# Kernel tuning notes

Hardware: AMD Instinct MI355X
Metric: run time of the kernel (lower is better)

Reference implementation:

```python
import jax, jax.numpy as jnp
import numpy as np

N, K, C_S, C_Z, C_G, NUM_RBF = 1024, 32, 384, 128, 16, 64
E = N * K


def _rbf(D):
    # GVP-style radial basis: D_min=0, D_max=20
    D_mu = jnp.linspace(0.0, 20.0, NUM_RBF)
    D_sigma = 20.0 / NUM_RBF
    return jnp.exp(-(((D[..., None] - D_mu) / D_sigma) ** 2))


def _ln(x, g, b, eps=1e-5):
    m = jnp.mean(x, axis=-1, keepdims=True)
    v = jnp.var(x, axis=-1, keepdims=True)
    return (x - m) * jax.lax.rsqrt(v + eps) * g + b


def setup_inputs() -> dict:
    key = jax.random.key(0)
    ks = jax.random.split(key, 16)
    w = lambda k, s: jax.random.normal(k, s, jnp.float32) / np.sqrt(s[0])
    # regular-degree graph: edges grouped by source node (what sparse_to_nested assumes)
    edge_index = jnp.stack([
        jnp.repeat(jnp.arange(N, dtype=jnp.int32), K),
        jax.random.randint(ks[3], (E,), 0, N, dtype=jnp.int32),
    ])
    return {
        "node_features": jax.random.normal(ks[0], (N, C_S), jnp.float32),
        "node_trans": 10.0 * jax.random.normal(ks[1], (N, 3), jnp.float32),
        "edge_features": jax.random.normal(ks[2], (E, C_Z), jnp.float32),
        "edge_index": edge_index,
        "W_nl": w(ks[4], (C_S, C_G)), "b_nl": jnp.zeros((C_G,), jnp.float32),
        "W_nr": w(ks[5], (C_S, C_G)), "b_nr": jnp.zeros((C_G,), jnp.float32),
        "ln_g": jnp.ones((C_Z,), jnp.float32), "ln_b": jnp.zeros((C_Z,), jnp.float32),
        "W_ep": w(ks[6], (C_Z, C_Z)), "b_ep": jnp.zeros((C_Z,), jnp.float32),
        "W_eg": w(ks[7], (C_Z, C_Z)), "b_eg": jnp.zeros((C_Z,), jnp.float32),
        "W_dg": w(ks[8], (C_G * C_G, C_Z)), "b_dg": jnp.zeros((C_Z,), jnp.float32),
        "W_dp": w(ks[9], (NUM_RBF, C_Z)), "b_dp": jnp.zeros((C_Z,), jnp.float32),
        "lno_g": jnp.ones((C_Z,), jnp.float32), "lno_b": jnp.zeros((C_Z,), jnp.float32),
        "W_lo": w(ks[10], (C_Z, C_Z)), "b_lo": jnp.zeros((C_Z,), jnp.float32),
        "W_og": w(ks[11], (C_Z, C_Z)), "b_og": jnp.zeros((C_Z,), jnp.float32),
    }


def reference(node_features, node_trans, edge_features, edge_index,
              W_nl, b_nl, W_nr, b_nr, ln_g, ln_b, W_ep, b_ep, W_eg, b_eg,
              W_dg, b_dg, W_dp, b_dp, lno_g, lno_b, W_lo, b_lo, W_og, b_og):
    n = node_features.shape[0]
    e = edge_index.shape[1]
    k = e // n
    cz = edge_features.shape[-1]
    eps = 1e-8
    nl = node_features @ W_nl + b_nl            # [N, cg]
    nr = node_features @ W_nr + b_nr            # [N, cg]
    # node_left[edge_index[0]] grouped by source node is constant within a group,
    # so edge3 = outer(nl[n], nr[n]) broadcast over (i, j)
    outer = nl[:, :, None] * nr[:, None, :]     # [N, cg, cg] ; flatten order = (a*cg + b)
    gate3 = jax.nn.sigmoid(outer.reshape(n, -1) @ W_dg + b_dg)   # [N, cz]
    dst = edge_index[1].reshape(n, k)           # [N, K]
    t = node_trans[dst]                         # [N, K, 3]
    diff = t[:, None, :, :] - t[:, :, None, :] + eps             # t[n,j] - t[n,i] + eps
    dist = jnp.sqrt(jnp.sum(diff * diff, axis=-1))               # [N, K, K]
    d3 = jnp.einsum('nijr,rz->nijz', _rbf(dist), W_dp) + b_dp    # [N, K, K, cz]
    e3 = gate3[:, None, None, :] * d3                            # sigmoid(dist_gate) * dist_proj
    ef = _ln(edge_features.reshape(n, k, cz), ln_g, ln_b)        # [N, K, cz]
    e2 = jax.nn.sigmoid(ef @ W_eg + b_eg) * (ef @ W_ep + b_ep)   # [N, K, cz]
    upd = jnp.einsum('nijz,njz->niz', e3, e2)                    # triangle multiply over j
    upd = _ln(upd, lno_g, lno_b) @ W_lo + b_lo
    upd = upd * jax.nn.sigmoid(ef @ W_og + b_og)                 # out gate
    return upd.reshape(e, cz)
```

## Files before the change

kernel.cpp:

```cpp
#include <hip/hip_runtime.h>

#define NN 1024
#define KK 32
#define CZ 128
#define CS 384
#define CG 16
#define NR 64

typedef __attribute__((ext_vector_type(8)))  _Float16 f16x8;
typedef __attribute__((ext_vector_type(16))) float    f32x16;

__device__ __forceinline__ float sigmoidf_(float x) { return 1.0f / (1.0f + __expf(-x)); }

__device__ __forceinline__ unsigned short h_bits(float f) {
    _Float16 h = (_Float16)f;
    return __builtin_bit_cast(unsigned short, h);
}
__device__ __forceinline__ float h2f_bits(unsigned short b) {
    return (float)__builtin_bit_cast(_Float16, b);
}

__launch_bounds__(256, 2)
__global__ void ntmu_kernel(
    const float* __restrict__ nf,
    const float* __restrict__ ntr,
    const float* __restrict__ efeat,
    const int*   __restrict__ eidx,
    const float* __restrict__ W_nl, const float* __restrict__ b_nl,
    const float* __restrict__ W_nr, const float* __restrict__ b_nr,
    const float* __restrict__ ln_g, const float* __restrict__ ln_b,
    const float* __restrict__ W_ep, const float* __restrict__ b_ep,
    const float* __restrict__ W_eg, const float* __restrict__ b_eg,
    const float* __restrict__ W_dg, const float* __restrict__ b_dg,
    const float* __restrict__ W_dp, const float* __restrict__ b_dp,
    const float* __restrict__ lno_g, const float* __restrict__ lno_b,
    const float* __restrict__ W_lo, const float* __restrict__ b_lo,
    const float* __restrict__ W_og, const float* __restrict__ b_og,
    float* __restrict__ out)
{
    const int n    = blockIdx.x;
    const int tid  = threadIdx.x;
    const int lane = tid & 63;
    const int wave = tid >> 6;
    const int hi   = lane >> 5;
    const int zt   = wave * 32;
    const int zc   = zt + (lane & 31);
    const int ebase = n * KK;

    __shared__ float s_e2 [KK*CZ];
    __shared__ float s_upd[KK*CZ];
    __shared__ short s_og [KK*CZ];
    __shared__ short s_ef [KK*CZ];
    __shared__ short s_updb[KK*CZ];
    __shared__ __align__(16) short s_T[4*KK*NR];
    __shared__ float s_t[KK][4];
    __shared__ float s_gate3[CZ];
    __shared__ float s_nl[CG], s_nr[CG];
    __shared__ float s_pp[2][CZ];

    if (tid < KK) {
        int d = eidx[NN*KK + ebase + tid];
        s_t[tid][0] = ntr[d*3 + 0];
        s_t[tid][1] = ntr[d*3 + 1];
        s_t[tid][2] = ntr[d*3 + 2];
    }
    if (wave < 2) {
        const float* W  = (wave == 0) ? W_nl : W_nr;
        const float* bb = (wave == 0) ? b_nl : b_nr;
        int g = lane >> 2, q = lane & 3;
        const float* x = nf + n * CS;
        float s = 0.f;
        int c0 = q * 96;
        for (int c = c0; c < c0 + 96; ++c) s = fmaf(x[c], W[c*CG + g], s);
        s += __shfl_xor(s, 1);
        s += __shfl_xor(s, 2);
        if (q == 0) { if (wave == 0) s_nl[g] = s + bb[g]; else s_nr[g] = s + bb[g]; }
    }
    __syncthreads();

    {
        int z = tid & 127, h = tid >> 7;
        float p = 0.f;
        for (int a = h*8; a < h*8 + 8; ++a) {
            float nla = s_nl[a];
            #pragma unroll
            for (int b = 0; b < 16; ++b)
                p = fmaf(nla * s_nr[b], W_dg[(a*16 + b)*CZ + z], p);
        }
        s_pp[h][z] = p;
    }

    {
        float g0 = ln_g[lane], g1 = ln_g[lane + 64];
        float bb0 = ln_b[lane], bb1 = ln_b[lane + 64];
        for (int it = 0; it < 8; ++it) {
            int j = it*4 + wave;
            const float* row = efeat + (ebase + j) * CZ;
            float x0 = row[lane], x1 = row[lane + 64];
            float s = x0 + x1, s2 = x0*x0 + x1*x1;
            #pragma unroll
            for (int o = 1; o < 64; o <<= 1) { s += __shfl_xor(s, o); s2 += __shfl_xor(s2, o); }
            float mu  = s * (1.f/128.f);
            float inv = rsqrtf(s2 * (1.f/128.f) - mu*mu + 1e-5f);
            float y0 = (x0 - mu) * inv * g0 + bb0;
            float y1 = (x1 - mu) * inv * g1 + bb1;
            int swz = (j & 7) << 4;
            *(short*)((char*)s_ef + ((j*256 + lane*2)        ^ swz)) = (short)h_bits(y0);
            *(short*)((char*)s_ef + ((j*256 + (lane+64)*2)   ^ swz)) = (short)h_bits(y1);
        }
    }
    __syncthreads();

    if (tid < CZ) s_gate3[tid] = sigmoidf_(s_pp[0][tid] + s_pp[1][tid] + b_dg[tid]);

    f32x16 aEp, aEg, aOg;
    #pragma unroll
    for (int r = 0; r < 16; ++r) { aEp[r] = 0.f; aEg[r] = 0.f; aOg[r] = 0.f; }
    {
        const int arow = lane & 31;
        const int aswz = (arow & 7) << 4;
        for (int ks = 0; ks < 8; ++ks) {
            int abyte = (arow*256 + ks*32 + hi*16) ^ aswz;
            f16x8 af = *reinterpret_cast<const f16x8*>((const char*)s_ef + abyte);
            int c0 = ks*16 + hi*8;
            const float* pep = W_ep + c0*CZ + zc;
            const float* peg = W_eg + c0*CZ + zc;
            const float* pog = W_og + c0*CZ + zc;
            f16x8 bep, beg, bog;
            #pragma unroll
            for (int t = 0; t < 8; ++t) {
                bep[t] = (_Float16)pep[t*CZ];
                beg[t] = (_Float16)peg[t*CZ];
                bog[t] = (_Float16)pog[t*CZ];
            }
            aEp = __builtin_amdgcn_mfma_f32_32x32x16_f16(af, bep, aEp, 0, 0, 0);
            aEg = __builtin_amdgcn_mfma_f32_32x32x16_f16(af, beg, aEg, 0, 0, 0);
            aOg = __builtin_amdgcn_mfma_f32_32x32x16_f16(af, bog, aOg, 0, 0, 0);
        }
    }
    float esum = 0.f;
    {
        float bep = b_ep[zc], beg = b_eg[zc], bogc = b_og[zc];
        #pragma unroll
        for (int r = 0; r < 16; ++r) {
            int j = (r & 3) + 8*(r >> 2) + 4*hi;
            float e2v = sigmoidf_(aEg[r] + beg) * (aEp[r] + bep);
            s_e2[j*CZ + zc] = e2v;
            esum += e2v;
            s_og[j*CZ + zc] = (short)h_bits(sigmoidf_(aOg[r] + bogc));
        }
        esum += __shfl_xor(esum, 32);
    }

    f16x8 wdp[4];
    #pragma unroll
    for (int ks = 0; ks < 4; ++ks) {
        int c0 = ks*16 + hi*8;
        const float* p = W_dp + c0*CZ + zc;
        #pragma unroll
        for (int t = 0; t < 8; ++t) wdp[ks][t] = (_Float16)p[t*CZ];
    }
    __syncthreads();
    const float g3  = s_gate3[zc];
    const float bdp = b_dp[zc];

    const float spacing     = 20.0f / 63.0f;
    const float inv_spacing = 63.0f / 20.0f;
    const float inv_sigma   = 64.0f / 20.0f;
    for (int ch = 0; ch < 8; ++ch) {
        __syncthreads();
        if (tid < 128) {
            int il = tid >> 5, j = tid & 31;
            int i  = ch*4 + il;
            float dx = s_t[j][0] - s_t[i][0] + 1e-8f;
            float dy = s_t[j][1] - s_t[i][1] + 1e-8f;
            float dz = s_t[j][2] - s_t[i][2] + 1e-8f;
            float D  = sqrtf(dx*dx + dy*dy + dz*dz);
            int idx = (int)(D * inv_spacing);
            int r0  = min(max((idx - 3) & ~1, 0), 56);
            int rowbyte = (il*KK + j) * 128;
            int swz = (j & 7) << 4;
            int4 zz; zz.x = 0; zz.y = 0; zz.z = 0; zz.w = 0;
            #pragma unroll
            for (int o = 0; o < 8; ++o)
                *reinterpret_cast<int4*>((char*)s_T + ((rowbyte + o*16) ^ swz)) = zz;
            #pragma unroll
            for (int w = 0; w < 4; ++w) {
                float mu0 = (float)(r0 + 2*w)     * spacing;
                float mu1 = (float)(r0 + 2*w + 1) * spacing;
                float d0 = (D - mu0) * inv_sigma;
                float d1 = (D - mu1) * inv_sigma;
                unsigned pk = (unsigned)h_bits(__expf(-d0*d0))
                            | ((unsigned)h_bits(__expf(-d1*d1)) << 16);
                *reinterpret_cast<unsigned*>((char*)s_T + ((rowbyte + r0*2 + w*4) ^ swz)) = pk;
            }
        }
        __syncthreads();
        const int arow = lane & 31;
        const int aswz = (arow & 7) << 4;
        #pragma unroll
        for (int il = 0; il < 4; ++il) {
            f32x16 acc;
            #pragma unroll
            for (int r = 0; r < 16; ++r) acc[r] = 0.f;
            int abase = (il*KK + arow) * 128 + hi*16;
            #pragma unroll
            for (int ks = 0; ks < 4; ++ks) {
                f16x8 af = *reinterpret_cast<const f16x8*>((const char*)s_T + ((abase + ks*32) ^ aswz));
                acc = __builtin_amdgcn_mfma_f32_32x32x16_f16(af, wdp[ks], acc, 0, 0, 0);
            }
            float sum = 0.f;
            #pragma unroll
            for (int r = 0; r < 16; ++r) {
                int j = (r & 3) + 8*(r >> 2) + 4*hi;
                sum = fmaf(acc[r], s_e2[j*CZ + zc], sum);
            }
            sum += __shfl_xor(sum, 32);
            if (lane < 32) s_upd[(ch*4 + il)*CZ + zc] = g3 * (sum + bdp * esum);
        }
    }
    __syncthreads();

    {
        float g0 = lno_g[lane], g1 = lno_g[lane + 64];
        float bb0 = lno_b[lane], bb1 = lno_b[lane + 64];
        for (int it = 0; it < 8; ++it) {
            int i = it*4 + wave;
            float x0 = s_upd[i*CZ + lane], x1 = s_upd[i*CZ + lane + 64];
            float s = x0 + x1, s2 = x0*x0 + x1*x1;
            #pragma unroll
            for (int o = 1; o < 64; o <<= 1) { s += __shfl_xor(s, o); s2 += __shfl_xor(s2, o); }
            float mu  = s * (1.f/128.f);
            float inv = rsqrtf(s2 * (1.f/128.f) - mu*mu + 1e-5f);
            float y0 = (x0 - mu) * inv * g0 + bb0;
            float y1 = (x1 - mu) * inv * g1 + bb1;
            int swz = (i & 7) << 4;
            *(short*)((char*)s_updb + ((i*256 + lane*2)      ^ swz)) = (short)h_bits(y0);
            *(short*)((char*)s_updb + ((i*256 + (lane+64)*2) ^ swz)) = (short)h_bits(y1);
        }
    }
    __syncthreads();

    {
        f32x16 aLo;
        #pragma unroll
        for (int r = 0; r < 16; ++r) aLo[r] = 0.f;
        const int arow = lane & 31;
        const int aswz = (arow & 7) << 4;
        for (int ks = 0; ks < 8; ++ks) {
            int abyte = (arow*256 + ks*32 + hi*16) ^ aswz;
            f16x8 af = *reinterpret_cast<const f16x8*>((const char*)s_updb + abyte);
            int c0 = ks*16 + hi*8;
            const float* plo = W_lo + c0*CZ + zc;
            f16x8 blo;
            #pragma unroll
            for (int t = 0; t < 8; ++t) blo[t] = (_Float16)plo[t*CZ];
            aLo = __builtin_amdgcn_mfma_f32_32x32x16_f16(af, blo, aLo, 0, 0, 0);
        }
        float bl = b_lo[zc];
        #pragma unroll
        for (int r = 0; r < 16; ++r) {
            int j = (r & 3) + 8*(r >> 2) + 4*hi;
            float og = h2f_bits((unsigned short)s_og[j*CZ + zc]);
            out[(ebase + j)*CZ + zc] = (aLo[r] + bl) * og;
        }
    }
}

extern "C" void kernel_launch(void* const* d_in, const int* in_sizes, int n_in,
                              void* d_out, int out_size, void* d_ws, size_t ws_size,
                              hipStream_t stream) {
    const float* nf    = (const float*)d_in[0];
    const float* ntr   = (const float*)d_in[1];
    const float* efeat = (const float*)d_in[2];
    const int*   eidx  = (const int*)  d_in[3];
    const float* W_nl  = (const float*)d_in[4];
    const float* b_nl  = (const float*)d_in[5];
    const float* W_nr  = (const float*)d_in[6];
    const float* b_nr  = (const float*)d_in[7];
    const float* ln_g  = (const float*)d_in[8];
    const float* ln_b  = (const float*)d_in[9];
    const float* W_ep  = (const float*)d_in[10];
    const float* b_ep  = (const float*)d_in[11];
    const float* W_eg  = (const float*)d_in[12];
    const float* b_eg  = (const float*)d_in[13];
    const float* W_dg  = (const float*)d_in[14];
    const float* b_dg  = (const float*)d_in[15];
    const float* W_dp  = (const float*)d_in[16];
    const float* b_dp  = (const float*)d_in[17];
    const float* lno_g = (const float*)d_in[18];
    const float* lno_b = (const float*)d_in[19];
    const float* W_lo  = (const float*)d_in[20];
    const float* b_lo  = (const float*)d_in[21];
    const float* W_og  = (const float*)d_in[22];
    const float* b_og  = (const float*)d_in[23];
    float* out = (float*)d_out;

    ntmu_kernel<<<NN, 256, 0, stream>>>(
        nf, ntr, efeat, eidx,
        W_nl, b_nl, W_nr, b_nr, ln_g, ln_b,
        W_ep, b_ep, W_eg, b_eg, W_dg, b_dg, W_dp, b_dp,
        lno_g, lno_b, W_lo, b_lo, W_og, b_og, out);
}
```

Baseline: 67.73 us.

## Pre-transpose weights to fp16 workspace, keep e2/og in registers, shrink LDS

Measured after the change: 66.29 us. 2.1% less time.

```diff
diff --git a/kernel.cpp b/kernel.cpp
--- a/kernel.cpp
+++ b/kernel.cpp
@@ -10,6 +10,15 @@
 typedef __attribute__((ext_vector_type(8)))  _Float16 f16x8;
 typedef __attribute__((ext_vector_type(16))) float    f32x16;
 
+#define WS_EP 0
+#define WS_EG 16384
+#define WS_OG 32768
+#define WS_LO 49152
+#define WS_DP 65536
+#define WS_NL 73728
+#define WS_NR 79872
+#define WS_TOT 86016
+
 __device__ __forceinline__ float sigmoidf_(float x) { return 1.0f / (1.0f + __expf(-x)); }
 
 __device__ __forceinline__ unsigned short h_bits(float f) {
@@ -20,22 +29,51 @@
     return (float)__builtin_bit_cast(_Float16, b);
 }
 
-__launch_bounds__(256, 2)
+__global__ void convert_weights(
+    const float* __restrict__ W_ep, const float* __restrict__ W_eg,
+    const float* __restrict__ W_og, const float* __restrict__ W_lo,
+    const float* __restrict__ W_dp, const float* __restrict__ W_nl,
+    const float* __restrict__ W_nr, _Float16* __restrict__ ws)
+{
+    int t = blockIdx.x * 256 + threadIdx.x;
+    if (t >= WS_TOT) return;
+    float v;
+    if (t < 65536) {
+        const float* src = (t < 16384) ? W_ep : (t < 32768) ? W_eg : (t < 49152) ? W_og : W_lo;
+        int tt = t & 16383;
+        int z = tt >> 7, c = tt & 127;
+        v = src[c*128 + z];
+    } else if (t < 73728) {
+        int tt = t - 65536;
+        int z = tt >> 6, r = tt & 63;
+        v = W_dp[r*128 + z];
+    } else if (t < 79872) {
+        int tt = t - 73728;
+        int g = tt / 384, c = tt - g*384;
+        v = W_nl[c*16 + g];
+    } else {
+        int tt = t - 79872;
+        int g = tt / 384, c = tt - g*384;
+        v = W_nr[c*16 + g];
+    }
+    ws[t] = (_Float16)v;
+}
+
+__launch_bounds__(256, 3)
 __global__ void ntmu_kernel(
     const float* __restrict__ nf,
     const float* __restrict__ ntr,
     const float* __restrict__ efeat,
     const int*   __restrict__ eidx,
-    const float* __restrict__ W_nl, const float* __restrict__ b_nl,
-    const float* __restrict__ W_nr, const float* __restrict__ b_nr,
-    const float* __restrict__ ln_g, const float* __restrict__ ln_b,
-    const float* __restrict__ W_ep, const float* __restrict__ b_ep,
-    const float* __restrict__ W_eg, const float* __restrict__ b_eg,
-    const float* __restrict__ W_dg, const float* __restrict__ b_dg,
-    const float* __restrict__ W_dp, const float* __restrict__ b_dp,
+    const float* __restrict__ W_dg,
+    const float* __restrict__ b_dg,
+    const float* __restrict__ ln_g,  const float* __restrict__ ln_b,
+    const float* __restrict__ b_nl,  const float* __restrict__ b_nr,
+    const float* __restrict__ b_ep,  const float* __restrict__ b_eg,
+    const float* __restrict__ b_og,  const float* __restrict__ b_dp,
     const float* __restrict__ lno_g, const float* __restrict__ lno_b,
-    const float* __restrict__ W_lo, const float* __restrict__ b_lo,
-    const float* __restrict__ W_og, const float* __restrict__ b_og,
+    const float* __restrict__ b_lo,
+    const _Float16* __restrict__ ws,
     float* __restrict__ out)
 {
     const int n    = blockIdx.x;
@@ -43,20 +81,20 @@
     const int lane = tid & 63;
     const int wave = tid >> 6;
     const int hi   = lane >> 5;
-    const int zt   = wave * 32;
-    const int zc   = zt + (lane & 31);
+    const int zc   = wave * 32 + (lane & 31);
+    const int arow = lane & 31;
+    const int aswz = (arow & 7) << 4;
     const int ebase = n * KK;
 
-    __shared__ float s_e2 [KK*CZ];
-    __shared__ float s_upd[KK*CZ];
-    __shared__ short s_og [KK*CZ];
-    __shared__ short s_ef [KK*CZ];
-    __shared__ short s_updb[KK*CZ];
-    __shared__ __align__(16) short s_T[4*KK*NR];
+    __shared__ __align__(16) short s_arena[8*KK*NR];
+    __shared__ short s_upd_h[KK*CZ];
     __shared__ float s_t[KK][4];
     __shared__ float s_gate3[CZ];
     __shared__ float s_nl[CG], s_nr[CG];
     __shared__ float s_pp[2][CZ];
+
+    short* s_ef = s_arena;
+    char*  s_T  = (char*)s_arena;
 
     if (tid < KK) {
         int d = eidx[NN*KK + ebase + tid];
@@ -65,22 +103,29 @@
         s_t[tid][2] = ntr[d*3 + 2];
     }
     if (wave < 2) {
-        const float* W  = (wave == 0) ? W_nl : W_nr;
-        const float* bb = (wave == 0) ? b_nl : b_nr;
         int g = lane >> 2, q = lane & 3;
-        const float* x = nf + n * CS;
+        const _Float16* Wt = ws + ((wave == 0) ? WS_NL : WS_NR) + g*384 + q*96;
+        const float* x = nf + n * CS + q*96;
         float s = 0.f;
-        int c0 = q * 96;
-        for (int c = c0; c < c0 + 96; ++c) s = fmaf(x[c], W[c*CG + g], s);
+        #pragma unroll
+        for (int c4 = 0; c4 < 96; c4 += 8) {
+            f16x8 wv = *reinterpret_cast<const f16x8*>(Wt + c4);
+            #pragma unroll
+            for (int t = 0; t < 8; ++t) s = fmaf(x[c4 + t], (float)wv[t], s);
+        }
         s += __shfl_xor(s, 1);
         s += __shfl_xor(s, 2);
-        if (q == 0) { if (wave == 0) s_nl[g] = s + bb[g]; else s_nr[g] = s + bb[g]; }
+        if (q == 0) {
+            if (wave == 0) s_nl[g] = s + b_nl[g];
+            else           s_nr[g] = s + b_nr[g];
+        }
     }
     __syncthreads();
 
     {
         int z = tid & 127, h = tid >> 7;
         float p = 0.f;
+        #pragma unroll 2
         for (int a = h*8; a < h*8 + 8; ++a) {
             float nla = s_nl[a];
             #pragma unroll
@@ -105,8 +150,8 @@
             float y0 = (x0 - mu) * inv * g0 + bb0;
             float y1 = (x1 - mu) * inv * g1 + bb1;
             int swz = (j & 7) << 4;
-            *(short*)((char*)s_ef + ((j*256 + lane*2)        ^ swz)) = (short)h_bits(y0);
-            *(short*)((char*)s_ef + ((j*256 + (lane+64)*2)   ^ swz)) = (short)h_bits(y1);
+            *(short*)((char*)s_ef + ((j*256 + lane*2)      ^ swz)) = (short)h_bits(y0);
+            *(short*)((char*)s_ef + ((j*256 + (lane+64)*2) ^ swz)) = (short)h_bits(y1);
         }
     }
     __syncthreads();
@@ -117,48 +162,42 @@
     #pragma unroll
     for (int r = 0; r < 16; ++r) { aEp[r] = 0.f; aEg[r] = 0.f; aOg[r] = 0.f; }
     {
-        const int arow = lane & 31;
-        const int aswz = (arow & 7) << 4;
+        const _Float16* wep = ws + WS_EP + zc*128;
+        const _Float16* weg = ws + WS_EG + zc*128;
+        const _Float16* wog = ws + WS_OG + zc*128;
+        #pragma unroll
         for (int ks = 0; ks < 8; ++ks) {
             int abyte = (arow*256 + ks*32 + hi*16) ^ aswz;
             f16x8 af = *reinterpret_cast<const f16x8*>((const char*)s_ef + abyte);
-            int c0 = ks*16 + hi*8;
-            const float* pep = W_ep + c0*CZ + zc;
-            const float* peg = W_eg + c0*CZ + zc;
-            const float* pog = W_og + c0*CZ + zc;
-            f16x8 bep, beg, bog;
-            #pragma unroll
-            for (int t = 0; t < 8; ++t) {
-                bep[t] = (_Float16)pep[t*CZ];
-                beg[t] = (_Float16)peg[t*CZ];
-                bog[t] = (_Float16)pog[t*CZ];
-            }
+            int kof = ks*16 + hi*8;
+            f16x8 bep = *reinterpret_cast<const f16x8*>(wep + kof);
+            f16x8 beg = *reinterpret_cast<const f16x8*>(weg + kof);
+            f16x8 bog = *reinterpret_cast<const f16x8*>(wog + kof);
             aEp = __builtin_amdgcn_mfma_f32_32x32x16_f16(af, bep, aEp, 0, 0, 0);
             aEg = __builtin_amdgcn_mfma_f32_32x32x16_f16(af, beg, aEg, 0, 0, 0);
             aOg = __builtin_amdgcn_mfma_f32_32x32x16_f16(af, bog, aOg, 0, 0, 0);
         }
     }
+    float e2v[16], og_r[16];
     float esum = 0.f;
     {
         float bep = b_ep[zc], beg = b_eg[zc], bogc = b_og[zc];
         #pragma unroll
         for (int r = 0; r < 16; ++r) {
-            int j = (r & 3) + 8*(r >> 2) + 4*hi;
-            float e2v = sigmoidf_(aEg[r] + beg) * (aEp[r] + bep);
-            s_e2[j*CZ + zc] = e2v;
-            esum += e2v;
-            s_og[j*CZ + zc] = (short)h_bits(sigmoidf_(aOg[r] + bogc));
+            float v = sigmoidf_(aEg[r] + beg) * (aEp[r] + bep);
+            e2v[r] = v;
+            esum += v;
+            og_r[r] = sigmoidf_(aOg[r] + bogc);
         }
         esum += __shfl_xor(esum, 32);
     }
 
     f16x8 wdp[4];
-    #pragma unroll
-    for (int ks = 0; ks < 4; ++ks) {
-        int c0 = ks*16 + hi*8;
-        const float* p = W_dp + c0*CZ + zc;
-        #pragma unroll
-        for (int t = 0; t < 8; ++t) wdp[ks][t] = (_Float16)p[t*CZ];
+    {
+        const _Float16* wdpp = ws + WS_DP + zc*64;
+        #pragma unroll
+        for (int ks = 0; ks < 4; ++ks)
+            wdp[ks] = *reinterpret_cast<const f16x8*>(wdpp + ks*16 + hi*8);
     }
     __syncthreads();
     const float g3  = s_gate3[zc];
@@ -167,66 +206,63 @@
     const float spacing     = 20.0f / 63.0f;
     const float inv_spacing = 63.0f / 20.0f;
     const float inv_sigma   = 64.0f / 20.0f;
-    for (int ch = 0; ch < 8; ++ch) {
-        __syncthreads();
-        if (tid < 128) {
-            int il = tid >> 5, j = tid & 31;
-            int i  = ch*4 + il;
+    for (int ch = 0; ch < 4; ++ch) {
+        {
+            int ilf = tid >> 5;
+            int j   = tid & 31;
+            int i   = ch*8 + ilf;
             float dx = s_t[j][0] - s_t[i][0] + 1e-8f;
             float dy = s_t[j][1] - s_t[i][1] + 1e-8f;
             float dz = s_t[j][2] - s_t[i][2] + 1e-8f;
             float D  = sqrtf(dx*dx + dy*dy + dz*dz);
             int idx = (int)(D * inv_spacing);
             int r0  = min(max((idx - 3) & ~1, 0), 56);
-            int rowbyte = (il*KK + j) * 128;
+            int rowbyte = (ilf*KK + j) * 128;
             int swz = (j & 7) << 4;
             int4 zz; zz.x = 0; zz.y = 0; zz.z = 0; zz.w = 0;
             #pragma unroll
             for (int o = 0; o < 8; ++o)
-                *reinterpret_cast<int4*>((char*)s_T + ((rowbyte + o*16) ^ swz)) = zz;
+                *reinterpret_cast<int4*>(s_T + ((rowbyte + o*16) ^ swz)) = zz;
             #pragma unroll
             for (int w = 0; w < 4; ++w) {
-                float mu0 = (float)(r0 + 2*w)     * spacing;
-                float mu1 = (float)(r0 + 2*w + 1) * spacing;
+                float mu0 = (float)(r0 + 2*w) * spacing;
+                float mu1 = mu0 + spacing;
                 float d0 = (D - mu0) * inv_sigma;
                 float d1 = (D - mu1) * inv_sigma;
                 unsigned pk = (unsigned)h_bits(__expf(-d0*d0))
                             | ((unsigned)h_bits(__expf(-d1*d1)) << 16);
-                *reinterpret_cast<unsigned*>((char*)s_T + ((rowbyte + r0*2 + w*4) ^ swz)) = pk;
+                *reinterpret_cast<unsigned*>(s_T + ((rowbyte + r0*2 + w*4) ^ swz)) = pk;
             }
         }
         __syncthreads();
-        const int arow = lane & 31;
-        const int aswz = (arow & 7) << 4;
-        #pragma unroll
-        for (int il = 0; il < 4; ++il) {
+        #pragma unroll
+        for (int il = 0; il < 8; ++il) {
             f32x16 acc;
             #pragma unroll
             for (int r = 0; r < 16; ++r) acc[r] = 0.f;
             int abase = (il*KK + arow) * 128 + hi*16;
             #pragma unroll
             for (int ks = 0; ks < 4; ++ks) {
-                f16x8 af = *reinterpret_cast<const f16x8*>((const char*)s_T + ((abase + ks*32) ^ aswz));
+                f16x8 af = *reinterpret_cast<const f16x8*>(s_T + ((abase + ks*32) ^ aswz));
                 acc = __builtin_amdgcn_mfma_f32_32x32x16_f16(af, wdp[ks], acc, 0, 0, 0);
             }
             float sum = 0.f;
             #pragma unroll
-            for (int r = 0; r < 16; ++r) {
-                int j = (r & 3) + 8*(r >> 2) + 4*hi;
-                sum = fmaf(acc[r], s_e2[j*CZ + zc], sum);
-            }
+            for (int r = 0; r < 16; ++r) sum = fmaf(acc[r], e2v[r], sum);
             sum += __shfl_xor(sum, 32);
-            if (lane < 32) s_upd[(ch*4 + il)*CZ + zc] = g3 * (sum + bdp * esum);
-        }
-    }
-    __syncthreads();
+            if (lane < 32)
+                s_upd_h[(ch*8 + il)*CZ + zc] = (short)h_bits(g3 * (sum + bdp * esum));
+        }
+        __syncthreads();
+    }
 
     {
         float g0 = lno_g[lane], g1 = lno_g[lane + 64];
         float bb0 = lno_b[lane], bb1 = lno_b[lane + 64];
         for (int it = 0; it < 8; ++it) {
             int i = it*4 + wave;
-            float x0 = s_upd[i*CZ + lane], x1 = s_upd[i*CZ + lane + 64];
+            float x0 = h2f_bits((unsigned short)s_upd_h[i*CZ + lane]);
+            float x1 = h2f_bits((unsigned short)s_upd_h[i*CZ + lane + 64]);
             float s = x0 + x1, s2 = x0*x0 + x1*x1;
             #pragma unroll
             for (int o = 1; o < 64; o <<= 1) { s += __shfl_xor(s, o); s2 += __shfl_xor(s2, o); }
@@ -235,8 +271,8 @@
             float y0 = (x0 - mu) * inv * g0 + bb0;
             float y1 = (x1 - mu) * inv * g1 + bb1;
             int swz = (i & 7) << 4;
-            *(short*)((char*)s_updb + ((i*256 + lane*2)      ^ swz)) = (short)h_bits(y0);
-            *(short*)((char*)s_updb + ((i*256 + (lane+64)*2) ^ swz)) = (short)h_bits(y1);
+            *(short*)((char*)s_upd_h + ((i*256 + lane*2)      ^ swz)) = (short)h_bits(y0);
+            *(short*)((char*)s_upd_h + ((i*256 + (lane+64)*2) ^ swz)) = (short)h_bits(y1);
         }
     }
     __syncthreads();
@@ -245,24 +281,19 @@
         f32x16 aLo;
         #pragma unroll
         for (int r = 0; r < 16; ++r) aLo[r] = 0.f;
-        const int arow = lane & 31;
-        const int aswz = (arow & 7) << 4;
+        const _Float16* wlo = ws + WS_LO + zc*128;
+        #pragma unroll
         for (int ks = 0; ks < 8; ++ks) {
             int abyte = (arow*256 + ks*32 + hi*16) ^ aswz;
-            f16x8 af = *reinterpret_cast<const f16x8*>((const char*)s_updb + abyte);
-            int c0 = ks*16 + hi*8;
-            const float* plo = W_lo + c0*CZ + zc;
-            f16x8 blo;
-            #pragma unroll
-            for (int t = 0; t < 8; ++t) blo[t] = (_Float16)plo[t*CZ];
+            f16x8 af = *reinterpret_cast<const f16x8*>((const char*)s_upd_h + abyte);
+            f16x8 blo = *reinterpret_cast<const f16x8*>(wlo + ks*16 + hi*8);
             aLo = __builtin_amdgcn_mfma_f32_32x32x16_f16(af, blo, aLo, 0, 0, 0);
         }
         float bl = b_lo[zc];
         #pragma unroll
         for (int r = 0; r < 16; ++r) {
             int j = (r & 3) + 8*(r >> 2) + 4*hi;
-            float og = h2f_bits((unsigned short)s_og[j*CZ + zc]);
-            out[(ebase + j)*CZ + zc] = (aLo[r] + bl) * og;
+            out[(ebase + j)*CZ + zc] = (aLo[r] + bl) * og_r[r];
         }
     }
 }
@@ -295,10 +326,14 @@
     const float* W_og  = (const float*)d_in[22];
     const float* b_og  = (const float*)d_in[23];
     float* out = (float*)d_out;
+    _Float16* ws = (_Float16*)d_ws;
+
+    convert_weights<<<(WS_TOT + 255)/256, 256, 0, stream>>>(
+        W_ep, W_eg, W_og, W_lo, W_dp, W_nl, W_nr, ws);
 
     ntmu_kernel<<<NN, 256, 0, stream>>>(
         nf, ntr, efeat, eidx,
-        W_nl, b_nl, W_nr, b_nr, ln_g, ln_b,
-        W_ep, b_ep, W_eg, b_eg, W_dg, b_dg, W_dp, b_dp,
-        lno_g, lno_b, W_lo, b_lo, W_og, b_og, out);
-}
+        W_dg, b_dg, ln_g, ln_b, b_nl, b_nr,
+        b_ep, b_eg, b_og, b_dp, lno_g, lno_b, b_lo,
+        ws, out);
+}
```
